# Optimization experiments

Hardware: AMD Instinct MI355X
Metric: run time of the kernel (lower is better)

The kernel has to match this reference:

```python
import jax, jax.numpy as jnp
import numpy as np

Q, N, D = 4096, 100000, 128


def setup_inputs() -> dict:
    key = jax.random.key(0)
    k1, k2, k3 = jax.random.split(key, 3)
    inputs = jax.random.normal(k1, (Q, D), dtype=jnp.float32)
    X_train = jax.random.normal(k2, (N, D), dtype=jnp.float32)
    y_train = jax.random.normal(k3, (N,), dtype=jnp.float32)
    return {"inputs": inputs, "X_train": X_train, "y_train": y_train, "k": 32}


def reference(inputs, X_train, y_train, k):
    # Squared Euclidean distances [Q, N] via the expanded identity
    # |a-b|^2 = |a|^2 + |b|^2 - 2 a.b  (avoids materializing [Q, N, D]).
    q_sq = jnp.sum(inputs * inputs, axis=-1, keepdims=True)        # [Q, 1]
    t_sq = jnp.sum(X_train * X_train, axis=-1)                     # [N]
    cross = jnp.einsum('qd,nd->qn', inputs, X_train)               # [Q, N]
    distances = q_sq + t_sq[None, :] - 2.0 * cross                 # [Q, N]
    # top_k of -distances == k nearest neighbors
    _, indices = jax.lax.top_k(-distances, k)                      # [Q, k]
    nearest = y_train[indices]                                     # [Q, k]
    return jnp.mean(nearest, axis=1)                               # [Q]
```

## Files before the change

kernel.cpp:

```cpp
#include <hip/hip_runtime.h>
#include <hip/hip_fp16.h>
#include <cstdint>
#include <cstddef>


constexpr int Q_  = 4096;
constexpr int N_  = 100000;
constexpr int D_  = 128;
constexpr int K_  = 32;

constexpr int QT    = 16;
constexpr int BN    = 256;
constexpr int NCH   = 8;
constexpr int CHUNK = 12544;
constexpr int ITERS = CHUNK / BN;
constexpr int NPAD  = NCH * CHUNK;
constexpr int CW    = 128;
constexpr int QTS   = 16;
constexpr int SAMP_M      = 8192;
constexpr int SAMP_STRIDE = 12;
constexpr int SAMP_OFF    = 5;
constexpr int SAMP_ITERS  = SAMP_M / BN;

constexpr int XS_B  = NPAD / 64;
constexpr int SAM_B = SAMP_M / 64;
constexpr int PQ_B  = Q_ / 4;
constexpr int MXN   = XS_B * 4;

typedef __attribute__((ext_vector_type(8))) _Float16 half8;
typedef __attribute__((ext_vector_type(4))) float    floatx4;
typedef unsigned long long ull;

#define DEV __device__ __forceinline__
constexpr ull DEADC = ~0ull;

DEV ull pack_cand(float score, unsigned int n) {
    unsigned int s = __float_as_uint(score);
    s = (s & 0x80000000u) ? ~s : (s | 0x80000000u);
    return ((ull)s << 32) | (ull)n;
}
DEV float unpack_score(ull k) {
    unsigned int s = (unsigned int)(k >> 32);
    s = (s & 0x80000000u) ? (s ^ 0x80000000u) : ~s;
    return __uint_as_float(s);
}
DEV ull u64min(ull a, ull b) { return a < b ? a : b; }
DEV float inf_f() { return __int_as_float(0x7f800000); }

DEV ull bitonic64(ull v, int L) {
    #pragma unroll
    for (int k2 = 2; k2 <= 64; k2 <<= 1)
        #pragma unroll
        for (int j2 = k2 >> 1; j2 >= 1; j2 >>= 1) {
            ull o = __shfl_xor(v, j2);
            bool up = ((L & k2) == 0);
            bool lo = ((L & j2) == 0);
            ull mn = u64min(v, o), mx = v ^ o ^ mn;
            v = (lo == up) ? mn : mx;
        }
    return v;
}
DEV ull bimerge64(ull v, int L) {
    #pragma unroll
    for (int j2 = 32; j2 >= 1; j2 >>= 1) {
        ull o = __shfl_xor(v, j2);
        ull mn = u64min(v, o), mx = v ^ o ^ mn;
        v = ((L & j2) == 0) ? mn : mx;
    }
    return v;
}

__global__ void prep_all(const float* __restrict__ X, const float* __restrict__ Qm,
                         __half* __restrict__ Xs, float* __restrict__ tsq,
                         float* __restrict__ mxArr,
                         __half* __restrict__ Xsam, float* __restrict__ tsqS,
                         __half* __restrict__ Qh, __half* __restrict__ Qr,
                         float* __restrict__ qsq, int* __restrict__ flagF)
{
    const int tid = threadIdx.x, L = tid & 63, wv = tid >> 6;
    const int bx = blockIdx.x;
    const int am = L & 15, aq = L >> 4;

    if (bx < XS_B) {
        int t16 = bx * 4 + wv;
        int r = t16 * 16 + am;
        float ssq = 0.f, xr2 = 0.f;
        #pragma unroll
        for (int ks = 0; ks < 4; ++ks) {
            int c = ks * 32 + aq * 8;
            float v0=0,v1=0,v2=0,v3=0,v4=0,v5=0,v6=0,v7=0;
            if (r < N_) {
                float4 a = *(const float4*)(X + (size_t)r * D_ + c);
                float4 b = *(const float4*)(X + (size_t)r * D_ + c + 4);
                v0=a.x; v1=a.y; v2=a.z; v3=a.w; v4=b.x; v5=b.y; v6=b.z; v7=b.w;
            }
            half8 h;
            h[0]=(_Float16)v0; h[1]=(_Float16)v1; h[2]=(_Float16)v2; h[3]=(_Float16)v3;
            h[4]=(_Float16)v4; h[5]=(_Float16)v5; h[6]=(_Float16)v6; h[7]=(_Float16)v7;
            float r0=v0-(float)h[0], r1=v1-(float)h[1], r2=v2-(float)h[2], r3=v3-(float)h[3];
            float r4=v4-(float)h[4], r5=v5-(float)h[5], r6=v6-(float)h[6], r7=v7-(float)h[7];
            ssq += v0*v0+v1*v1+v2*v2+v3*v3+v4*v4+v5*v5+v6*v6+v7*v7;
            xr2 += r0*r0+r1*r1+r2*r2+r3*r3+r4*r4+r5*r5+r6*r6+r7*r7;
            *(half8*)(Xs + ((size_t)(t16 * 4 + ks)) * 512 + L * 8) = h;
        }
        ssq += __shfl_xor(ssq, 16); ssq += __shfl_xor(ssq, 32);
        xr2 += __shfl_xor(xr2, 16); xr2 += __shfl_xor(xr2, 32);
        if (aq == 0) tsq[r] = (r < N_) ? ssq : inf_f();
        float m = xr2;
        m = fmaxf(m, __shfl_xor(m, 1)); m = fmaxf(m, __shfl_xor(m, 2));
        m = fmaxf(m, __shfl_xor(m, 4)); m = fmaxf(m, __shfl_xor(m, 8));
        if (L == 0) mxArr[t16] = m;
    } else if (bx < XS_B + SAM_B) {
        int t16 = (bx - XS_B) * 4 + wv;
        int j = t16 * 16 + am;
        int n = j * SAMP_STRIDE + SAMP_OFF;
        float ssq = 0.f;
        #pragma unroll
        for (int ks = 0; ks < 4; ++ks) {
            int c = ks * 32 + aq * 8;
            float4 a = *(const float4*)(X + (size_t)n * D_ + c);
            float4 b = *(const float4*)(X + (size_t)n * D_ + c + 4);
            half8 h;
            h[0]=(_Float16)a.x; h[1]=(_Float16)a.y; h[2]=(_Float16)a.z; h[3]=(_Float16)a.w;
            h[4]=(_Float16)b.x; h[5]=(_Float16)b.y; h[6]=(_Float16)b.z; h[7]=(_Float16)b.w;
            ssq += a.x*a.x + a.y*a.y + a.z*a.z + a.w*a.w
                 + b.x*b.x + b.y*b.y + b.z*b.z + b.w*b.w;
            *(half8*)(Xsam + ((size_t)(t16 * 4 + ks)) * 512 + L * 8) = h;
        }
        ssq += __shfl_xor(ssq, 16); ssq += __shfl_xor(ssq, 32);
        if (aq == 0) tsqS[j] = ssq;
    } else {
        int r = (bx - XS_B - SAM_B) * 4 + wv;
        float2 x = *(const float2*)(Qm + (size_t)r * D_ + 2 * L);
        __half h0 = __float2half(x.x), h1 = __float2half(x.y);
        size_t o = (size_t)r * D_ + 2 * L;
        Qh[o] = h0; Qh[o + 1] = h1;
        Qr[o]     = __float2half(x.x - __half2float(h0));
        Qr[o + 1] = __float2half(x.y - __half2float(h1));
        float s = x.x * x.x + x.y * x.y;
        s += __shfl_xor(s, 32); s += __shfl_xor(s, 16); s += __shfl_xor(s, 8);
        s += __shfl_xor(s, 4);  s += __shfl_xor(s, 2);  s += __shfl_xor(s, 1);
        if (L == 0) { qsq[r] = s; flagF[r] = 0; }
    }
}

__global__ __launch_bounds__(256, 2) void sample_T(
    const __half* __restrict__ Qh, const __half* __restrict__ Qr,
    const __half* __restrict__ Xsam, const float* __restrict__ tsqS,
    const float* __restrict__ qsq, const float* __restrict__ mxArr,
    float* __restrict__ Teff, float* __restrict__ rawT, float* __restrict__ EwA)
{
    __shared__ float sT[QTS][130];
    const int tid = threadIdx.x, L = tid & 63, wv = tid >> 6;
    const int qbase = blockIdx.x * QTS;
    const int nwv = wv * 64;
    const int am = L & 15, aq = L >> 4;

    half8 afh[4], afr[4];
    #pragma unroll
    for (int ks = 0; ks < 4; ++ks) {
        size_t o = (size_t)(qbase + am) * D_ + ks * 32 + aq * 8;
        afh[ks] = *(const half8*)(Qh + o);
        afr[ks] = *(const half8*)(Qr + o);
    }

    float t2a[4], t2b[4];
    #pragma unroll
    for (int rg = 0; rg < 4; ++rg) { t2a[rg] = inf_f(); t2b[rg] = inf_f(); }

    const __half* bp = Xsam + (size_t)nwv * 128 + (size_t)L * 8;
    const float*  tp = tsqS + nwv + am;

    half8 bc[4], bn[4];
    #pragma unroll
    for (int nt = 0; nt < 4; ++nt)
        bc[nt] = *(const half8*)(bp + nt * 2048);

    #pragma unroll 1
    for (int it = 0; it < SAMP_ITERS; ++it) {
        float ts[4];
        #pragma unroll
        for (int nt = 0; nt < 4; ++nt) ts[nt] = tp[nt * 16];

        floatx4 acc[4] = {};
        #pragma unroll
        for (int ks = 0; ks < 4; ++ks) {
            const __half* pp = (ks < 3) ? (bp + (ks + 1) * 512) : (bp + 32768);
            #pragma unroll
            for (int nt = 0; nt < 4; ++nt)
                bn[nt] = *(const half8*)(pp + nt * 2048);
            #pragma unroll
            for (int nt = 0; nt < 4; ++nt) {
                acc[nt] = __builtin_amdgcn_mfma_f32_16x16x32_f16(
                    afh[ks], bc[nt], acc[nt], 0, 0, 0);
                acc[nt] = __builtin_amdgcn_mfma_f32_16x16x32_f16(
                    afr[ks], bc[nt], acc[nt], 0, 0, 0);
            }
            #pragma unroll
            for (int nt = 0; nt < 4; ++nt) bc[nt] = bn[nt];
        }
        #pragma unroll
        for (int rg = 0; rg < 4; ++rg) {
            float m1 = t2a[rg], m2 = t2b[rg];
            #pragma unroll
            for (int nt = 0; nt < 4; ++nt) {
                float v = ts[nt] - 2.f * acc[nt][rg];
                if (v < m2) { if (v < m1) { m2 = m1; m1 = v; } else m2 = v; }
            }
            t2a[rg] = m1; t2b[rg] = m2;
        }
        bp += 32768; tp += BN;
    }
    #pragma unroll
    for (int rg = 0; rg < 4; ++rg) {
        int q = aq * 4 + rg;
        sT[q][wv * 32 + am * 2 + 0] = t2a[rg];
        sT[q][wv * 32 + am * 2 + 1] = t2b[rg];
    }
    __syncthreads();

    float mxr = 0.f;
    #pragma unroll 1
    for (int i = L; i < MXN; i += 64) mxr = fmaxf(mxr, mxArr[i]);
    mxr = fmaxf(mxr, __shfl_xor(mxr, 32)); mxr = fmaxf(mxr, __shfl_xor(mxr, 16));
    mxr = fmaxf(mxr, __shfl_xor(mxr, 8));  mxr = fmaxf(mxr, __shfl_xor(mxr, 4));
    mxr = fmaxf(mxr, __shfl_xor(mxr, 2));  mxr = fmaxf(mxr, __shfl_xor(mxr, 1));

    #pragma unroll 1
    for (int j = 0; j < 4; ++j) {
        int q = wv * 4 + j;
        float a = sT[q][2 * L], b = sT[q][2 * L + 1];
        float g = 0.f;
        #pragma unroll 1
        for (int r = 0; r < 16; ++r) {
            float mn = fminf(a, b);
            mn = fminf(mn, __shfl_xor(mn, 32)); mn = fminf(mn, __shfl_xor(mn, 16));
            mn = fminf(mn, __shfl_xor(mn, 8));  mn = fminf(mn, __shfl_xor(mn, 4));
            mn = fminf(mn, __shfl_xor(mn, 2));  mn = fminf(mn, __shfl_xor(mn, 1));
            g = mn;
            ull ba = __ballot(a == g);
            if (ba) { if (L == __ffsll(ba) - 1) a = inf_f(); }
            else    { ull bb = __ballot(b == g); if (L == __ffsll(bb) - 1) b = inf_f(); }
        }
        if (L == 0) {
            int gq = qbase + q;
            float e = 2.f * sqrtf(qsq[gq]) * sqrtf(mxr) + 0.02f;
            rawT[gq] = g; EwA[gq] = e; Teff[gq] = g + e;
        }
    }
}

__global__ __launch_bounds__(256, 4) void knn_main(
    const __half* __restrict__ Qh, const __half* __restrict__ Qr,
    const __half* __restrict__ Xs, const float* __restrict__ tsq,
    const float* __restrict__ Teff, ull* __restrict__ candG,
    int* __restrict__ cntC, int* __restrict__ flagF)
{
    __shared__ ull candL[QT][CW];
    __shared__ int cntL[QT];

    const int tid = threadIdx.x, L = tid & 63, wv = tid >> 6;
    const int lb = blockIdx.x, ch = lb & 7;
    const int qbase = (lb >> 3) * QT, chBase = ch * CHUNK, nwv = wv * 64;
    const int am = L & 15, aq = L >> 4;

    if (tid < QT) cntL[tid] = 0;
    __syncthreads();

    float th[4];
    #pragma unroll
    for (int rg = 0; rg < 4; ++rg)
        th[rg] = Teff[qbase + aq * 4 + rg];
    float maxTh = fmaxf(fmaxf(th[0], th[1]), fmaxf(th[2], th[3]));
    const float negHalfMaxTh = -0.5f * maxTh - 1e-3f;

    half8 afh[4], afr[4];
    #pragma unroll
    for (int ks = 0; ks < 4; ++ks) {
        size_t o = (size_t)(qbase + am) * D_ + ks * 32 + aq * 8;
        afh[ks] = *(const half8*)(Qh + o);
        afr[ks] = *(const half8*)(Qr + o);
    }

    const __half* bp = Xs + (size_t)(chBase + nwv) * 128 + (size_t)L * 8;
    const float*  tp = tsq + chBase + nwv + am;
    int n0 = chBase + nwv + am;

    half8 bc[4], bn[4];
    #pragma unroll
    for (int nt = 0; nt < 4; ++nt)
        bc[nt] = *(const half8*)(bp + nt * 2048);

    #pragma unroll 1
    for (int it = 0; it < ITERS; ++it) {
        float ts[4];
        #pragma unroll
        for (int nt = 0; nt < 4; ++nt) ts[nt] = tp[nt * 16];

        floatx4 acc[4] = {};
        #pragma unroll
        for (int ks = 0; ks < 4; ++ks) {
            const __half* pp = (ks < 3) ? (bp + (ks + 1) * 512) : (bp + 32768);
            #pragma unroll
            for (int nt = 0; nt < 4; ++nt)
                bn[nt] = *(const half8*)(pp + nt * 2048);
            #pragma unroll
            for (int nt = 0; nt < 4; ++nt) {
                acc[nt] = __builtin_amdgcn_mfma_f32_16x16x32_f16(
                    afh[ks], bc[nt], acc[nt], 0, 0, 0);
                acc[nt] = __builtin_amdgcn_mfma_f32_16x16x32_f16(
                    afr[ks], bc[nt], acc[nt], 0, 0, 0);
            }
            #pragma unroll
            for (int nt = 0; nt < 4; ++nt) bc[nt] = bn[nt];
        }

        unsigned hit = 0;
        #pragma unroll
        for (int nt = 0; nt < 4; ++nt) {
            float mx = fmaxf(fmaxf(acc[nt][0], acc[nt][1]),
                             fmaxf(acc[nt][2], acc[nt][3]));
            float Gm = fmaf(0.5f, ts[nt], negHalfMaxTh);
            if (mx > Gm) hit |= 1u << nt;
        }
        if (__any(hit != 0)) {
            #pragma unroll
            for (int nt = 0; nt < 4; ++nt) {
                if (!__any(hit & (1u << nt))) continue;
                unsigned n = (unsigned)(n0 + nt * 16);
                #pragma unroll
                for (int rg = 0; rg < 4; ++rg) {
                    float s = fmaf(-2.f, acc[nt][rg], ts[nt]);
                    if (s < th[rg]) {
                        int q = aq * 4 + rg;
                        int pos = atomicAdd(&cntL[q], 1);
                        if (pos < CW)
                            candL[q][pos] = pack_cand(s, n);
                        else
                            flagF[qbase + q] = 1;
                    }
                }
            }
        }
        bp += 32768; tp += BN; n0 += BN;
    }

    __syncthreads();

    #pragma unroll 1
    for (int j = 0; j < 4; ++j) {
        int q = wv * 4 + j;
        int gq = qbase + q;
        int c = cntL[q];
        int cc = c < CW ? c : CW;
        ull* dst = candG + ((size_t)gq * NCH + ch) * CW;
        #pragma unroll
        for (int off = 0; off < CW; off += 64)
            if (off + L < cc) dst[off + L] = candL[q][off + L];
        if (L == 0) cntC[gq * NCH + ch] = cc;
    }
}

__global__ void finalize(const ull* __restrict__ candG, const int* __restrict__ cntC,
                         const int* __restrict__ flagF, const float* __restrict__ Qm,
                         const float* __restrict__ X, const float* __restrict__ tsq,
                         const float* __restrict__ rawT, const float* __restrict__ EwA,
                         const float* __restrict__ Ytr, float* __restrict__ out)
{
    __shared__ ull fb[4][256];
    int L = threadIdx.x & 63;
    int wv = threadIdx.x >> 6;
    int q = blockIdx.x * 4 + wv;
    bool bad = (flagF[q] != 0);
    float result = 0.f;

    if (!bad) {
        int cg = (L < NCH) ? cntC[q * NCH + L] : 0;
        int ctot = cg;
        ctot += __shfl_xor(ctot, 32); ctot += __shfl_xor(ctot, 16);
        ctot += __shfl_xor(ctot, 8);  ctot += __shfl_xor(ctot, 4);
        ctot += __shfl_xor(ctot, 2);  ctot += __shfl_xor(ctot, 1);
        if (ctot < K_) bad = true;
        else {
            ull s = DEADC;
            #pragma unroll 1
            for (int g = 0; g < NCH; ++g) {
                int c_g = __shfl(cg, g);
                const ull* cb = candG + ((size_t)q * NCH + g) * CW;
                #pragma unroll 1
                for (int off = 0; off < c_g; off += 64) {
                    ull v = (off + L < c_g) ? cb[off + L] : DEADC;
                    v = bitonic64(v, L);
                    ull w = __shfl(v, 63 - L);
                    s = bimerge64(u64min(s, w), L);
                }
            }
            int cr = ctot < 64 ? ctot : 64;
            unsigned n = (unsigned)(s & 0xffffffffu);
            ull pe = DEADC;
            if (L < cr) {
                const float4* xp = (const float4*)(X + (size_t)n * D_);
                const float4* qp = (const float4*)(Qm + (size_t)q * D_);
                float d = 0.f;
                #pragma unroll 8
                for (int i = 0; i < 32; ++i) {
                    float4 xv = xp[i], qv = qp[i];
                    d += qv.x * xv.x + qv.y * xv.y + qv.z * xv.z + qv.w * xv.w;
                }
                pe = pack_cand(tsq[n] - 2.f * d, n);
            }
            ull pe2 = bitonic64(pe, L);
            float exact31 = unpack_score(__shfl(pe2, K_ - 1));
            bool ok = exact31 < rawT[q];
            if (ctot > 64) {
                float A63 = unpack_score(__shfl(s, 63));
                ok = ok && (A63 - EwA[q] > exact31);
            }
            if (!ok) bad = true;
            else {
                float ys = 0.f;
                if (L < K_) ys = Ytr[(unsigned)(pe2 & 0xffffffffu)];
                ys += __shfl_xor(ys, 32); ys += __shfl_xor(ys, 16);
                ys += __shfl_xor(ys, 8);  ys += __shfl_xor(ys, 4);
                ys += __shfl_xor(ys, 2);  ys += __shfl_xor(ys, 1);
                result = ys * (1.f / K_);
            }
        }
    }

    if (bad) {
        const float4* qp = (const float4*)(Qm + (size_t)q * D_);
        float T = rawT[q] + EwA[q];
        float lo = 0.f, hi = 0.f;
        bool haveLo = false, haveHi = false;
        int cnt = 0;
        #pragma unroll 1
        for (int att = 0; att < 40; ++att) {
            cnt = 0;
            #pragma unroll 1
            for (int j = 0; j < NPAD / 64; ++j) {
                int n = j * 64 + L;
                float s = inf_f();
                if (n < N_) {
                    const float4* xp = (const float4*)(X + (size_t)n * D_);
                    float d = 0.f;
                    #pragma unroll 4
                    for (int i = 0; i < 32; ++i) {
                        float4 xv = xp[i], qv = qp[i];
                        d += qv.x * xv.x + qv.y * xv.y + qv.z * xv.z + qv.w * xv.w;
                    }
                    s = tsq[n] - 2.f * d;
                }
                bool want = s < T;
                ull m = __ballot(want);
                if (m) {
                    int pos = cnt + (int)__popcll(m & ((1ull << L) - 1ull));
                    if (want && pos < 256) fb[wv][pos] = pack_cand(s, (unsigned)n);
                    cnt += (int)__popcll(m);
                }
            }
            if (cnt >= K_ && cnt <= 256) break;
            if (cnt < K_) { lo = T; haveLo = true;
                T = haveHi ? 0.5f * (T + hi) : T + exp2f((float)att) * 0.5f; }
            else { hi = T; haveHi = true;
                T = haveLo ? 0.5f * (lo + T) : T - exp2f((float)att) * 0.5f; }
        }
        if (cnt >= K_ && cnt <= 256) {
            ull s64 = DEADC;
            #pragma unroll 1
            for (int off = 0; off < 256; off += 64) {
                if (off >= cnt) break;
                ull v = (off + L < cnt) ? fb[wv][off + L] : DEADC;
                v = bitonic64(v, L);
                ull w = __shfl(v, 63 - L);
                s64 = bimerge64(u64min(s64, w), L);
            }
            float ys = (L < K_) ? Ytr[(unsigned)(s64 & 0xffffffffu)] : 0.f;
            ys += __shfl_xor(ys, 32); ys += __shfl_xor(ys, 16);
            ys += __shfl_xor(ys, 8);  ys += __shfl_xor(ys, 4);
            ys += __shfl_xor(ys, 2);  ys += __shfl_xor(ys, 1);
            result = ys * (1.f / K_);
        } else {
            ull last = 0;
            float ysum = 0.f;
            for (int r = 0; r < K_; ++r) {
                ull best = DEADC;
                for (int j = 0; j < NPAD / 64; ++j) {
                    int n = j * 64 + L;
                    if (n < N_) {
                        const float4* xp = (const float4*)(X + (size_t)n * D_);
                        float d = 0.f;
                        #pragma unroll 4
                        for (int i = 0; i < 32; ++i) {
                            float4 xv = xp[i], qv = qp[i];
                            d += qv.x * xv.x + qv.y * xv.y + qv.z * xv.z + qv.w * xv.w;
                        }
                        ull k = pack_cand(tsq[n] - 2.f * d, n);
                        if (k > last && k < best) best = k;
                    }
                }
                best = u64min(best, __shfl_xor(best, 32));
                best = u64min(best, __shfl_xor(best, 16));
                best = u64min(best, __shfl_xor(best, 8));
                best = u64min(best, __shfl_xor(best, 4));
                best = u64min(best, __shfl_xor(best, 2));
                best = u64min(best, __shfl_xor(best, 1));
                if (L == 0) ysum += Ytr[(unsigned)(best & 0xffffffffu)];
                last = best;
            }
            result = ysum * (1.f / K_);
        }
    }
    if (L == 0) out[q] = result;
}

extern "C" void kernel_launch(void* const* d_in, const int* in_sizes, int n_in,
                              void* d_out, int out_size, void* d_ws, size_t ws_size,
                              hipStream_t stream)
{
    const float* Qm  = (const float*)d_in[0];
    const float* X   = (const float*)d_in[1];
    const float* Ytr = (const float*)d_in[2];
    float* out = (float*)d_out;

    char* w = (char*)d_ws;
    auto alloc = [&](size_t bytes) {
        char* p = w; w += (bytes + 255) & ~(size_t)255; return p;
    };
    __half* Xs   = (__half*)  alloc((size_t)(NPAD + BN) * D_ * 2);
    __half* Qh   = (__half*)  alloc((size_t)Q_ * D_ * 2);
    __half* Qr   = (__half*)  alloc((size_t)Q_ * D_ * 2);
    float*  ts   = (float*)   alloc((size_t)NPAD * 4);
    __half* Xsm  = (__half*)  alloc((size_t)(SAMP_M + BN) * D_ * 2);
    float*  tsS  = (float*)   alloc((size_t)SAMP_M * 4);
    ull*    cd   = (ull*)     alloc((size_t)Q_ * NCH * CW * 8);
    int*    cnC  = (int*)     alloc((size_t)Q_ * NCH * 4);
    int*    flg  = (int*)     alloc((size_t)Q_ * 4);
    float*  mxA  = (float*)   alloc((size_t)MXN * 4);
    float*  Tef  = (float*)   alloc((size_t)Q_ * 4);
    float*  rwT  = (float*)   alloc((size_t)Q_ * 4);
    float*  Ew   = (float*)   alloc((size_t)Q_ * 4);
    float*  qs   = (float*)   alloc((size_t)Q_ * 4);

    prep_all<<<XS_B + SAM_B + PQ_B, 256, 0, stream>>>(
        X, Qm, Xs, ts, mxA, Xsm, tsS, Qh, Qr, qs, flg);
    sample_T<<<Q_ / QTS, 256, 0, stream>>>(Qh, Qr, Xsm, tsS, qs, mxA, Tef, rwT, Ew);
    knn_main<<<(Q_ / QT) * NCH, 256, 0, stream>>>(Qh, Qr, Xs, ts, Tef, cd, cnC, flg);
    finalize<<<Q_ / 4, 256, 0, stream>>>(cd, cnC, flg, Qm, X, ts, rwT, Ew, Ytr, out);
}
```

Before: 479.0 us.

## Process two 16-query tiles per block to reuse streamed X_train fragments

Each knn_main block now handles 32 queries instead of 16 by keeping two sets of query A-fragments and accumulators, so every X_train B-fragment loaded from global memory feeds twice as many MFMAs. This halves the number of blocks and total X_train traffic. The cost is higher register pressure, reflected in lowering launch bounds occupancy from 4 to 3, doubled shared candidate buffers, and fewer blocks in the grid.

```diff
diff --git a/kernel.cpp b/kernel.cpp
--- a/kernel.cpp
+++ b/kernel.cpp
@@ -9,7 +9,7 @@
 constexpr int D_  = 128;
 constexpr int K_  = 32;
 
-constexpr int QT    = 16;
+constexpr int QT    = 32;
 constexpr int BN    = 256;
 constexpr int NCH   = 8;
 constexpr int CHUNK = 12544;
@@ -250,7 +250,7 @@
     }
 }
 
-__global__ __launch_bounds__(256, 4) void knn_main(
+__global__ __launch_bounds__(256, 3) void knn_main(
     const __half* __restrict__ Qh, const __half* __restrict__ Qr,
     const __half* __restrict__ Xs, const float* __restrict__ tsq,
     const float* __restrict__ Teff, ull* __restrict__ candG,
@@ -267,20 +267,26 @@
     if (tid < QT) cntL[tid] = 0;
     __syncthreads();
 
-    float th[4];
-    #pragma unroll
-    for (int rg = 0; rg < 4; ++rg)
-        th[rg] = Teff[qbase + aq * 4 + rg];
-    float maxTh = fmaxf(fmaxf(th[0], th[1]), fmaxf(th[2], th[3]));
-    const float negHalfMaxTh = -0.5f * maxTh - 1e-3f;
-
-    half8 afh[4], afr[4];
-    #pragma unroll
-    for (int ks = 0; ks < 4; ++ks) {
-        size_t o = (size_t)(qbase + am) * D_ + ks * 32 + aq * 8;
-        afh[ks] = *(const half8*)(Qh + o);
-        afr[ks] = *(const half8*)(Qr + o);
-    }
+    float th[2][4];
+    float nhm[2];
+    #pragma unroll
+    for (int qt = 0; qt < 2; ++qt) {
+        #pragma unroll
+        for (int rg = 0; rg < 4; ++rg)
+            th[qt][rg] = Teff[qbase + qt * 16 + aq * 4 + rg];
+        float m = fmaxf(fmaxf(th[qt][0], th[qt][1]), fmaxf(th[qt][2], th[qt][3]));
+        nhm[qt] = -0.5f * m - 1e-3f;
+    }
+
+    half8 afh[2][4], afr[2][4];
+    #pragma unroll
+    for (int qt = 0; qt < 2; ++qt)
+        #pragma unroll
+        for (int ks = 0; ks < 4; ++ks) {
+            size_t o = (size_t)(qbase + qt * 16 + am) * D_ + ks * 32 + aq * 8;
+            afh[qt][ks] = *(const half8*)(Qh + o);
+            afr[qt][ks] = *(const half8*)(Qr + o);
+        }
 
     const __half* bp = Xs + (size_t)(chBase + nwv) * 128 + (size_t)L * 8;
     const float*  tp = tsq + chBase + nwv + am;
@@ -297,7 +303,7 @@
         #pragma unroll
         for (int nt = 0; nt < 4; ++nt) ts[nt] = tp[nt * 16];
 
-        floatx4 acc[4] = {};
+        floatx4 acc[2][4] = {};
         #pragma unroll
         for (int ks = 0; ks < 4; ++ks) {
             const __half* pp = (ks < 3) ? (bp + (ks + 1) * 512) : (bp + 32768);
@@ -305,39 +311,47 @@
             for (int nt = 0; nt < 4; ++nt)
                 bn[nt] = *(const half8*)(pp + nt * 2048);
             #pragma unroll
+            for (int nt = 0; nt < 4; ++nt)
+                #pragma unroll
+                for (int qt = 0; qt < 2; ++qt) {
+                    acc[qt][nt] = __builtin_amdgcn_mfma_f32_16x16x32_f16(
+                        afh[qt][ks], bc[nt], acc[qt][nt], 0, 0, 0);
+                    acc[qt][nt] = __builtin_amdgcn_mfma_f32_16x16x32_f16(
+                        afr[qt][ks], bc[nt], acc[qt][nt], 0, 0, 0);
+                }
+            #pragma unroll
+            for (int nt = 0; nt < 4; ++nt) bc[nt] = bn[nt];
+        }
+
+        unsigned hit = 0;
+        #pragma unroll
+        for (int qt = 0; qt < 2; ++qt)
+            #pragma unroll
             for (int nt = 0; nt < 4; ++nt) {
-                acc[nt] = __builtin_amdgcn_mfma_f32_16x16x32_f16(
-                    afh[ks], bc[nt], acc[nt], 0, 0, 0);
-                acc[nt] = __builtin_amdgcn_mfma_f32_16x16x32_f16(
-                    afr[ks], bc[nt], acc[nt], 0, 0, 0);
-            }
-            #pragma unroll
-            for (int nt = 0; nt < 4; ++nt) bc[nt] = bn[nt];
-        }
-
-        unsigned hit = 0;
-        #pragma unroll
-        for (int nt = 0; nt < 4; ++nt) {
-            float mx = fmaxf(fmaxf(acc[nt][0], acc[nt][1]),
-                             fmaxf(acc[nt][2], acc[nt][3]));
-            float Gm = fmaf(0.5f, ts[nt], negHalfMaxTh);
-            if (mx > Gm) hit |= 1u << nt;
-        }
+                float mx = fmaxf(fmaxf(acc[qt][nt][0], acc[qt][nt][1]),
+                                 fmaxf(acc[qt][nt][2], acc[qt][nt][3]));
+                float Gm = fmaf(0.5f, ts[nt], nhm[qt]);
+                if (mx > Gm) hit |= 1u << (qt * 4 + nt);
+            }
         if (__any(hit != 0)) {
             #pragma unroll
-            for (int nt = 0; nt < 4; ++nt) {
-                if (!__any(hit & (1u << nt))) continue;
-                unsigned n = (unsigned)(n0 + nt * 16);
+            for (int qt = 0; qt < 2; ++qt) {
+                if (!__any((hit >> (qt * 4)) & 0xfu)) continue;
                 #pragma unroll
-                for (int rg = 0; rg < 4; ++rg) {
-                    float s = fmaf(-2.f, acc[nt][rg], ts[nt]);
-                    if (s < th[rg]) {
-                        int q = aq * 4 + rg;
-                        int pos = atomicAdd(&cntL[q], 1);
-                        if (pos < CW)
-                            candL[q][pos] = pack_cand(s, n);
-                        else
-                            flagF[qbase + q] = 1;
+                for (int nt = 0; nt < 4; ++nt) {
+                    if (!__any(hit & (1u << (qt * 4 + nt)))) continue;
+                    unsigned n = (unsigned)(n0 + nt * 16);
+                    #pragma unroll
+                    for (int rg = 0; rg < 4; ++rg) {
+                        float s = fmaf(-2.f, acc[qt][nt][rg], ts[nt]);
+                        if (s < th[qt][rg]) {
+                            int q = qt * 16 + aq * 4 + rg;
+                            int pos = atomicAdd(&cntL[q], 1);
+                            if (pos < CW)
+                                candL[q][pos] = pack_cand(s, n);
+                            else
+                                flagF[qbase + q] = 1;
+                        }
                     }
                 }
             }
@@ -348,8 +362,8 @@
     __syncthreads();
 
     #pragma unroll 1
-    for (int j = 0; j < 4; ++j) {
-        int q = wv * 4 + j;
+    for (int j = 0; j < 8; ++j) {
+        int q = wv * 8 + j;
         int gq = qbase + q;
         int c = cntL[q];
         int cc = c < CW ? c : CW;
```

After: 571.5 us. +19.3%, slower.

## Give each knn_main wave its own query group and share X tiles across waves

Applied to the files above, without the earlier changes.

Changes the knn_main work split: each block now covers 64 queries, with each wave owning 16 of them and all four waves walking the same 64-point X slices, instead of 16 shared queries with waves splitting the points. Waves in a block now load the same X data, which is meant to get reuse through cache and quarter the number of blocks streaming X per query group. The block-wide barriers go away because each wave touches only its own candidate rows in shared memory. The cost is a larger per-block shared candidate buffer, a drop in occupancy hint from 4 to 2 blocks, and 4x fewer blocks in the grid, which may hurt latency hiding.

```diff
diff --git a/kernel.cpp b/kernel.cpp
--- a/kernel.cpp
+++ b/kernel.cpp
@@ -9,18 +9,19 @@
 constexpr int D_  = 128;
 constexpr int K_  = 32;
 
-constexpr int QT    = 16;
-constexpr int BN    = 256;
+constexpr int QT    = 64;
+constexpr int BNM   = 64;
 constexpr int NCH   = 8;
 constexpr int CHUNK = 12544;
-constexpr int ITERS = CHUNK / BN;
+constexpr int ITERS = CHUNK / BNM;
 constexpr int NPAD  = NCH * CHUNK;
 constexpr int CW    = 128;
 constexpr int QTS   = 16;
+constexpr int SBN   = 256;
 constexpr int SAMP_M      = 8192;
 constexpr int SAMP_STRIDE = 12;
 constexpr int SAMP_OFF    = 5;
-constexpr int SAMP_ITERS  = SAMP_M / BN;
+constexpr int SAMP_ITERS  = SAMP_M / SBN;
 
 constexpr int XS_B  = NPAD / 64;
 constexpr int SAM_B = SAMP_M / 64;
@@ -209,7 +210,7 @@
             }
             t2a[rg] = m1; t2b[rg] = m2;
         }
-        bp += 32768; tp += BN;
+        bp += 32768; tp += SBN;
     }
     #pragma unroll
     for (int rg = 0; rg < 4; ++rg) {
@@ -250,7 +251,7 @@
     }
 }
 
-__global__ __launch_bounds__(256, 4) void knn_main(
+__global__ __launch_bounds__(256, 2) void knn_main(
     const __half* __restrict__ Qh, const __half* __restrict__ Qr,
     const __half* __restrict__ Xs, const float* __restrict__ tsq,
     const float* __restrict__ Teff, ull* __restrict__ candG,
@@ -261,30 +262,30 @@
 
     const int tid = threadIdx.x, L = tid & 63, wv = tid >> 6;
     const int lb = blockIdx.x, ch = lb & 7;
-    const int qbase = (lb >> 3) * QT, chBase = ch * CHUNK, nwv = wv * 64;
+    const int qbase = (lb >> 3) * QT, chBase = ch * CHUNK;
     const int am = L & 15, aq = L >> 4;
-
-    if (tid < QT) cntL[tid] = 0;
-    __syncthreads();
+    const int qw = qbase + wv * 16;
+
+    if (L < 16) cntL[wv * 16 + L] = 0;
 
     float th[4];
     #pragma unroll
     for (int rg = 0; rg < 4; ++rg)
-        th[rg] = Teff[qbase + aq * 4 + rg];
+        th[rg] = Teff[qw + aq * 4 + rg];
     float maxTh = fmaxf(fmaxf(th[0], th[1]), fmaxf(th[2], th[3]));
     const float negHalfMaxTh = -0.5f * maxTh - 1e-3f;
 
     half8 afh[4], afr[4];
     #pragma unroll
     for (int ks = 0; ks < 4; ++ks) {
-        size_t o = (size_t)(qbase + am) * D_ + ks * 32 + aq * 8;
+        size_t o = (size_t)(qw + am) * D_ + ks * 32 + aq * 8;
         afh[ks] = *(const half8*)(Qh + o);
         afr[ks] = *(const half8*)(Qr + o);
     }
 
-    const __half* bp = Xs + (size_t)(chBase + nwv) * 128 + (size_t)L * 8;
-    const float*  tp = tsq + chBase + nwv + am;
-    int n0 = chBase + nwv + am;
+    const __half* bp = Xs + (size_t)chBase * 128 + (size_t)L * 8;
+    const float*  tp = tsq + chBase + am;
+    int n0 = chBase + am;
 
     half8 bc[4], bn[4];
     #pragma unroll
@@ -300,7 +301,7 @@
         floatx4 acc[4] = {};
         #pragma unroll
         for (int ks = 0; ks < 4; ++ks) {
-            const __half* pp = (ks < 3) ? (bp + (ks + 1) * 512) : (bp + 32768);
+            const __half* pp = (ks < 3) ? (bp + (ks + 1) * 512) : (bp + 8192);
             #pragma unroll
             for (int nt = 0; nt < 4; ++nt)
                 bn[nt] = *(const half8*)(pp + nt * 2048);
@@ -332,7 +333,7 @@
                 for (int rg = 0; rg < 4; ++rg) {
                     float s = fmaf(-2.f, acc[nt][rg], ts[nt]);
                     if (s < th[rg]) {
-                        int q = aq * 4 + rg;
+                        int q = wv * 16 + aq * 4 + rg;
                         int pos = atomicAdd(&cntL[q], 1);
                         if (pos < CW)
                             candL[q][pos] = pack_cand(s, n);
@@ -342,14 +343,12 @@
                 }
             }
         }
-        bp += 32768; tp += BN; n0 += BN;
-    }
-
-    __syncthreads();
+        bp += 8192; tp += BNM; n0 += BNM;
+    }
 
     #pragma unroll 1
-    for (int j = 0; j < 4; ++j) {
-        int q = wv * 4 + j;
+    for (int j = 0; j < 16; ++j) {
+        int q = wv * 16 + j;
         int gq = qbase + q;
         int c = cntL[q];
         int cc = c < CW ? c : CW;
@@ -527,11 +526,11 @@
     auto alloc = [&](size_t bytes) {
         char* p = w; w += (bytes + 255) & ~(size_t)255; return p;
     };
-    __half* Xs   = (__half*)  alloc((size_t)(NPAD + BN) * D_ * 2);
+    __half* Xs   = (__half*)  alloc((size_t)(NPAD + 256) * D_ * 2);
     __half* Qh   = (__half*)  alloc((size_t)Q_ * D_ * 2);
     __half* Qr   = (__half*)  alloc((size_t)Q_ * D_ * 2);
     float*  ts   = (float*)   alloc((size_t)NPAD * 4);
-    __half* Xsm  = (__half*)  alloc((size_t)(SAMP_M + BN) * D_ * 2);
+    __half* Xsm  = (__half*)  alloc((size_t)(SAMP_M + 256) * D_ * 2);
     float*  tsS  = (float*)   alloc((size_t)SAMP_M * 4);
     ull*    cd   = (ull*)     alloc((size_t)Q_ * NCH * CW * 8);
     int*    cnC  = (int*)     alloc((size_t)Q_ * NCH * 4);
```

New measurement: 484.3 us. No clear change (+1.1%).
